# Kernel tuning notes

Hardware: AMD Instinct MI355X
Metric: run time of the kernel (lower is better)

## Reference

```python
import jax, jax.numpy as jnp
import numpy as np

B, L, D, H, NBLK, NNBR = 256, 200, 128, 2, 2, 10
ITEMS, USERS = 100001, 50001
NEG = -1e9
EPS = 1e-8


def layernorm(x, s, b):
    mu = jnp.mean(x, axis=-1, keepdims=True)
    var = jnp.mean(jnp.square(x - mu), axis=-1, keepdims=True)
    return (x - mu) / jnp.sqrt(var + EPS) * s + b


def mha(q, kv, Wqkv_i, bqkv_i, Wo_i, bo_i, causal_bias):
    # torch.nn.MultiheadAttention math (eval mode), Q from layernormed seq, K=V=seq
    d = q.shape[-1]
    hd = d // H
    Wq, Wk, Wv = Wqkv_i[:d], Wqkv_i[d:2 * d], Wqkv_i[2 * d:]
    bq, bk, bv = bqkv_i[:d], bqkv_i[d:2 * d], bqkv_i[2 * d:]
    Q = (q @ Wq.T + bq).reshape(q.shape[0], q.shape[1], H, hd)
    K = (kv @ Wk.T + bk).reshape(q.shape[0], q.shape[1], H, hd)
    V = (kv @ Wv.T + bv).reshape(q.shape[0], q.shape[1], H, hd)
    scores = jnp.einsum('bqhd,bkhd->bhqk', Q, K) / jnp.sqrt(jnp.float32(hd))
    attn = jax.nn.softmax(scores + causal_bias, axis=-1)
    out = jnp.einsum('bhqk,bkhd->bqhd', attn, V).reshape(q.shape[0], q.shape[1], d)
    return out @ Wo_i.T + bo_i


def setup_inputs() -> dict:
    key = jax.random.key(0)
    ks = jax.random.split(key, 12)
    s = 0.02
    inp = {
        'log_seqs': jax.random.randint(ks[0], (B, L), 0, ITEMS),
        'nbr_idx': jax.random.randint(ks[1], (B, L, NNBR), 0, USERS),
        'item_emb': jax.random.normal(ks[2], (ITEMS, D), jnp.float32) * s,
        'user_emb': jax.random.normal(ks[3], (USERS, D), jnp.float32) * s,
        'pos_emb': jax.random.normal(ks[4], (L, D), jnp.float32) * s,
        'attn_ln_s': jnp.ones((NBLK, D), jnp.float32),
        'attn_ln_b': jnp.zeros((NBLK, D), jnp.float32),
        'Wqkv': jax.random.normal(ks[5], (NBLK, 3 * D, D), jnp.float32) * s,
        'bqkv': jnp.zeros((NBLK, 3 * D), jnp.float32),
        'Wo': jax.random.normal(ks[6], (NBLK, D, D), jnp.float32) * s,
        'bo': jnp.zeros((NBLK, D), jnp.float32),
        'ffn_ln_s': jnp.ones((NBLK, D), jnp.float32),
        'ffn_ln_b': jnp.zeros((NBLK, D), jnp.float32),
        'W1': jax.random.normal(ks[7], (NBLK, D, D), jnp.float32) * s,
        'b1': jnp.zeros((NBLK, D), jnp.float32),
        'W2': jax.random.normal(ks[8], (NBLK, D, D), jnp.float32) * s,
        'b2': jnp.zeros((NBLK, D), jnp.float32),
        'last_ln_s': jnp.ones((D,), jnp.float32),
        'last_ln_b': jnp.zeros((D,), jnp.float32),
        'iui_ln_s': jnp.ones((D,), jnp.float32),
        'iui_ln_b': jnp.zeros((D,), jnp.float32),
    }
    return inp


def reference(log_seqs, nbr_idx, item_emb, user_emb, pos_emb, attn_ln_s, attn_ln_b,
              Wqkv, bqkv, Wo, bo, ffn_ln_s, ffn_ln_b, W1, b1, W2, b2,
              last_ln_s, last_ln_b, iui_ln_s, iui_ln_b):
    d = item_emb.shape[1]
    seqlen = log_seqs.shape[1]
    # SASRec log2feats core (eval mode, dropout disabled)
    seqs = item_emb[log_seqs] * jnp.sqrt(jnp.float32(d)) + pos_emb[None, :seqlen]
    tl_mask = (log_seqs != 0)[..., None].astype(seqs.dtype)
    seqs = seqs * tl_mask
    causal_bias = jnp.where(jnp.tril(jnp.ones((seqlen, seqlen), bool)), 0.0, NEG)
    for i in range(Wqkv.shape[0]):
        q = layernorm(seqs, attn_ln_s[i], attn_ln_b[i])
        seqs = q + mha(q, seqs, Wqkv[i], bqkv[i], Wo[i], bo[i], causal_bias)
        x = layernorm(seqs, ffn_ln_s[i], ffn_ln_b[i])
        # PointWiseFeedForward: 1x1 conv == linear, residual inside
        h = jax.nn.relu(x @ W1[i].T + b1[i]) @ W2[i].T + b2[i]
        seqs = (h + x) * tl_mask
    feats = layernorm(seqs, last_ln_s, last_ln_b)
    # iui meta-path: gather up to 10 user neighbors per item, masked attention aggregation
    qn = item_emb[log_seqs]                       # [B,L,D]
    kn = user_emb[nbr_idx]                        # [B,L,N,D]
    sc = jnp.einsum('bld,blnd->bln', qn, kn) / jnp.sqrt(jnp.float32(d))
    sc = jnp.where(nbr_idx != 0, sc, NEG)
    w = jax.nn.softmax(sc, axis=-1)
    agg = jnp.einsum('bln,blnd->bld', w, kn)
    nbr = layernorm(agg + qn, iui_ln_s, iui_ln_b)
    return feats + nbr
```

## Files before the change

kernel.cpp:

```cpp
#include <hip/hip_runtime.h>
#include <hip/hip_bf16.h>

#define L_SEQ 200
#define DIM 128
#define NROWS (256*200)

typedef __attribute__((ext_vector_type(8))) short bf16x8;
typedef __attribute__((ext_vector_type(4))) float f32x4;

__device__ __forceinline__ float wave_sum(float v){
  #pragma unroll
  for (int o = 32; o; o >>= 1) v += __shfl_xor(v, o);
  return v;
}
__device__ __forceinline__ short f2bf(float f){
  union { float f; unsigned u; } x; x.f = f;
  unsigned r = x.u + 0x7fffu + ((x.u >> 16) & 1u);
  return (short)(r >> 16);
}
__device__ __forceinline__ float bf2f(unsigned short u){
  union { unsigned u; float f; } x; x.u = ((unsigned)u) << 16;
  return x.f;
}

__global__ void cvt_all_kernel(const float* __restrict__ Wqkv, const float* __restrict__ Wo,
                               const float* __restrict__ W1, const float* __restrict__ W2,
                               short* __restrict__ dst){
  int i = blockIdx.x*256 + threadIdx.x;
  if (i >= 49152) return;
  const float* src; int off;
  if (i < 24576)      { src = Wqkv; off = i; }
  else if (i < 32768) { src = Wo;   off = i - 24576; }
  else if (i < 40960) { src = W1;   off = i - 32768; }
  else                { src = W2;   off = i - 40960; }
  float4 v = ((const float4*)src)[off];
  short4 s; s.x = f2bf(v.x); s.y = f2bf(v.y); s.z = f2bf(v.z); s.w = f2bf(v.w);
  ((short4*)dst)[i] = s;
}

__global__ void cvt4_kernel(const float* __restrict__ src, short* __restrict__ dst, int n4){
  int i = blockIdx.x*256 + threadIdx.x;
  if (i < n4) {
    float4 v = ((const float4*)src)[i];
    short4 s; s.x = f2bf(v.x); s.y = f2bf(v.y); s.z = f2bf(v.z); s.w = f2bf(v.w);
    ((short4*)dst)[i] = s;
  }
}

__global__ __launch_bounds__(256) void embed_ln_kernel(
    const int* __restrict__ lsq, const float* __restrict__ item,
    const float* __restrict__ pos, const float* __restrict__ s, const float* __restrict__ b,
    short* __restrict__ seqs_b, short* __restrict__ lnq_b, short* __restrict__ qn_b){
  int wave = threadIdx.x >> 6, lane = threadIdx.x & 63;
  size_t r = (size_t)blockIdx.x*4 + wave;
  int it = lsq[r];
  float2 iv = ((const float2*)(item + (size_t)it*DIM))[lane];
  float2 p = ((const float2*)(pos + (r % L_SEQ)*DIM))[lane];
  short2 qv; qv.x = f2bf(iv.x); qv.y = f2bf(iv.y);
  ((short2*)(qn_b + r*DIM))[lane] = qv;
  float vx = 0.f, vy = 0.f;
  if (it) {
    vx = iv.x * 11.313708498984761f + p.x;
    vy = iv.y * 11.313708498984761f + p.y;
  }
  short2 sv; sv.x = f2bf(vx); sv.y = f2bf(vy);
  ((short2*)(seqs_b + r*DIM))[lane] = sv;
  float mu = wave_sum(vx + vy) * (1.f/DIM);
  float dx = vx - mu, dy = vy - mu;
  float var = wave_sum(dx*dx + dy*dy) * (1.f/DIM);
  float inv = 1.f / sqrtf(var + 1e-8f);
  float2 sc = ((const float2*)s)[lane];
  float2 bc = ((const float2*)b)[lane];
  short2 ov; ov.x = f2bf(dx*inv*sc.x + bc.x); ov.y = f2bf(dy*inv*sc.y + bc.y);
  ((short2*)(lnq_b + r*DIM))[lane] = ov;
}

#define MLP_MFMA(accv) do { \
  _Pragma("unroll") \
  for (int kc = 0; kc < 4; ++kc) { \
    bf16x8 af[4], bfr[2]; \
    _Pragma("unroll") \
    for (int mf = 0; mf < 4; ++mf) { \
      int rr = mbase + mf*16 + col; \
      int byt = (rr*256 + kc*64 + g*16) ^ ((rr & 7) << 4); \
      af[mf] = *(bf16x8*)(AsB + byt); \
    } \
    _Pragma("unroll") \
    for (int nf = 0; nf < 2; ++nf) { \
      int rr = nbase + nf*16 + col; \
      int byt = (rr*256 + kc*64 + g*16) ^ ((rr & 7) << 4); \
      bfr[nf] = *(bf16x8*)(BsB + byt); \
    } \
    _Pragma("unroll") \
    for (int mf = 0; mf < 4; ++mf) \
      _Pragma("unroll") \
      for (int nf = 0; nf < 2; ++nf) \
        accv[mf][nf] = __builtin_amdgcn_mfma_f32_16x16x32_bf16(af[mf], bfr[nf], accv[mf][nf], 0, 0, 0); \
  } \
} while(0)

#define LN_REDUCE(accv) do { \
  _Pragma("unroll") \
  for (int mf = 0; mf < 4; ++mf) { \
    _Pragma("unroll") \
    for (int r = 0; r < 4; ++r) { \
      float s1 = accv[mf][0][r] + accv[mf][1][r]; \
      float s2 = accv[mf][0][r]*accv[mf][0][r] + accv[mf][1][r]*accv[mf][1][r]; \
      _Pragma("unroll") \
      for (int o = 1; o <= 8; o <<= 1) { s1 += __shfl_xor(s1, o); s2 += __shfl_xor(s2, o); } \
      if (col == 0) { int rL = mbase + mf*16 + g*4 + r; redP[0][wn][rL] = s1; redP[1][wn][rL] = s2; } \
    } \
  } \
  __syncthreads(); \
  if (t < 128) { \
    float s1 = redP[0][0][t] + redP[0][1][t] + redP[0][2][t] + redP[0][3][t]; \
    float s2 = redP[1][0][t] + redP[1][1][t] + redP[1][2][t] + redP[1][3][t]; \
    float mu_ = s1 * (1.f/DIM); \
    float var_ = s2 * (1.f/DIM) - mu_*mu_; \
    muA[t] = mu_; invA[t] = 1.f / sqrtf(var_ + 1e-8f); \
  } \
  __syncthreads(); \
} while(0)

__global__ __launch_bounds__(512) void qkv_kernel(
    const short* __restrict__ lnq, const short* __restrict__ seqs,
    const short* __restrict__ Wb, const float* __restrict__ bias,
    short* __restrict__ C){
  __shared__ short As[16384];
  __shared__ short Bs[16384];
  char* AsB = (char*)As; char* BsB = (char*)Bs;
  const int row0 = blockIdx.y * 128, col0 = blockIdx.x * 128;
  const int t = threadIdx.x;
  const short* Ap = (blockIdx.x == 0) ? lnq : seqs;

  #pragma unroll
  for (int i = 0; i < 4; ++i) {
    int flat = t*8 + i*4096;
    int rr = flat >> 7, cc = flat & 127;
    bf16x8 a8 = *(const bf16x8*)(Ap + (size_t)(row0 + rr)*128 + cc);
    int byt = (rr*256 + cc*2) ^ ((rr & 7) << 4);
    *(bf16x8*)(AsB + byt) = a8;
    bf16x8 b8 = *(const bf16x8*)(Wb + (size_t)(col0 + rr)*128 + cc);
    *(bf16x8*)(BsB + byt) = b8;
  }
  __syncthreads();

  const int w = t >> 6, l = t & 63;
  const int wm = w >> 2, wn = w & 3;
  const int col = l & 15, g = l >> 4;
  const int mbase = wm*64, nbase = wn*32;

  f32x4 acc[4][2];
  #pragma unroll
  for (int mf = 0; mf < 4; ++mf)
    #pragma unroll
    for (int nf = 0; nf < 2; ++nf) { f32x4 z = {0.f,0.f,0.f,0.f}; acc[mf][nf] = z; }
  MLP_MFMA(acc);

  float biasv[2];
  #pragma unroll
  for (int nf = 0; nf < 2; ++nf) biasv[nf] = bias[col0 + nbase + nf*16 + col];
  const float qs = (blockIdx.x == 0) ? 0.125f : 1.f;
  #pragma unroll
  for (int mf = 0; mf < 4; ++mf)
    #pragma unroll
    for (int r = 0; r < 4; ++r) {
      int rr = row0 + mbase + mf*16 + g*4 + r;
      #pragma unroll
      for (int nf = 0; nf < 2; ++nf) {
        int cc = col0 + nbase + nf*16 + col;
        float v = (acc[mf][nf][r] + biasv[nf]) * qs;
        C[(size_t)rr*384 + cc] = f2bf(v);
      }
    }
}

template<int WRITE_C>
__global__ __launch_bounds__(512) void mlp_kernel(
    const short* __restrict__ qkvQ, const short* __restrict__ resq,
    const short* __restrict__ wo_b, const float* __restrict__ bo,
    const float* __restrict__ ffnS, const float* __restrict__ ffnB,
    const short* __restrict__ w1_b, const float* __restrict__ b1,
    const short* __restrict__ w2_b, const float* __restrict__ b2,
    const int* __restrict__ lsq,
    short* __restrict__ C,
    const float* __restrict__ lnS2, const float* __restrict__ lnB2,
    short* __restrict__ lnOut){
  __shared__ short As[16384];
  __shared__ short Bs[16384];
  __shared__ float redP[2][4][128];
  __shared__ float muA[128], invA[128];
  char* AsB = (char*)As; char* BsB = (char*)Bs;
  const int row0 = blockIdx.x * 128;
  const int t = threadIdx.x;

  #pragma unroll
  for (int i = 0; i < 4; ++i) {
    int flat = t*8 + i*4096;
    int rr = flat >> 7, cc = flat & 127;
    bf16x8 a8 = *(const bf16x8*)(qkvQ + (size_t)(row0 + rr)*384 + cc);
    int byt = (rr*256 + cc*2) ^ ((rr & 7) << 4);
    *(bf16x8*)(AsB + byt) = a8;
    bf16x8 b8 = *(const bf16x8*)(wo_b + (size_t)rr*128 + cc);
    *(bf16x8*)(BsB + byt) = b8;
  }
  __syncthreads();

  const int w = t >> 6, l = t & 63;
  const int wm = w >> 2, wn = w & 3;
  const int col = l & 15, g = l >> 4;
  const int mbase = wm*64, nbase = wn*32;

  f32x4 acc[4][2];
  #pragma unroll
  for (int mf = 0; mf < 4; ++mf)
    #pragma unroll
    for (int nf = 0; nf < 2; ++nf) { f32x4 z = {0.f,0.f,0.f,0.f}; acc[mf][nf] = z; }
  MLP_MFMA(acc);

  float bov[2];
  #pragma unroll
  for (int nf = 0; nf < 2; ++nf) bov[nf] = bo[nbase + nf*16 + col];
  #pragma unroll
  for (int mf = 0; mf < 4; ++mf)
    #pragma unroll
    for (int r = 0; r < 4; ++r) {
      int rL = mbase + mf*16 + g*4 + r;
      #pragma unroll
      for (int nf = 0; nf < 2; ++nf) {
        int cL = nbase + nf*16 + col;
        acc[mf][nf][r] += bov[nf] + bf2f(((const unsigned short*)resq)[(size_t)(row0 + rL)*DIM + cL]);
      }
    }
  LN_REDUCE(acc);

  float xv[4][2][4];
  #pragma unroll
  for (int mf = 0; mf < 4; ++mf)
    #pragma unroll
    for (int r = 0; r < 4; ++r) {
      int rL = mbase + mf*16 + g*4 + r;
      float mu = muA[rL], inv = invA[rL];
      #pragma unroll
      for (int nf = 0; nf < 2; ++nf) {
        int cL = nbase + nf*16 + col;
        float lnv = (acc[mf][nf][r] - mu)*inv*ffnS[cL] + ffnB[cL];
        xv[mf][nf][r] = lnv;
        int byt = (rL*256 + cL*2) ^ ((rL & 7) << 4);
        *(short*)(AsB + byt) = f2bf(lnv);
      }
    }
  #pragma unroll
  for (int i = 0; i < 4; ++i) {
    int flat = t*8 + i*4096;
    int rr = flat >> 7, cc = flat & 127;
    bf16x8 b8 = *(const bf16x8*)(w1_b + (size_t)rr*128 + cc);
    int byt = (rr*256 + cc*2) ^ ((rr & 7) << 4);
    *(bf16x8*)(BsB + byt) = b8;
  }
  __syncthreads();

  #pragma unroll
  for (int mf = 0; mf < 4; ++mf)
    #pragma unroll
    for (int nf = 0; nf < 2; ++nf) { f32x4 z = {0.f,0.f,0.f,0.f}; acc[mf][nf] = z; }
  MLP_MFMA(acc);
  __syncthreads();

  float b1v[2];
  #pragma unroll
  for (int nf = 0; nf < 2; ++nf) b1v[nf] = b1[nbase + nf*16 + col];
  #pragma unroll
  for (int mf = 0; mf < 4; ++mf)
    #pragma unroll
    for (int r = 0; r < 4; ++r) {
      int rL = mbase + mf*16 + g*4 + r;
      #pragma unroll
      for (int nf = 0; nf < 2; ++nf) {
        int cL = nbase + nf*16 + col;
        float h = fmaxf(acc[mf][nf][r] + b1v[nf], 0.f);
        int byt = (rL*256 + cL*2) ^ ((rL & 7) << 4);
        *(short*)(AsB + byt) = f2bf(h);
      }
    }
  #pragma unroll
  for (int i = 0; i < 4; ++i) {
    int flat = t*8 + i*4096;
    int rr = flat >> 7, cc = flat & 127;
    bf16x8 b8 = *(const bf16x8*)(w2_b + (size_t)rr*128 + cc);
    int byt = (rr*256 + cc*2) ^ ((rr & 7) << 4);
    *(bf16x8*)(BsB + byt) = b8;
  }
  __syncthreads();

  #pragma unroll
  for (int mf = 0; mf < 4; ++mf)
    #pragma unroll
    for (int nf = 0; nf < 2; ++nf) { f32x4 z = {0.f,0.f,0.f,0.f}; acc[mf][nf] = z; }
  MLP_MFMA(acc);

  float b2v[2];
  #pragma unroll
  for (int nf = 0; nf < 2; ++nf) b2v[nf] = b2[nbase + nf*16 + col];
  #pragma unroll
  for (int mf = 0; mf < 4; ++mf)
    #pragma unroll
    for (int r = 0; r < 4; ++r) {
      int rL = mbase + mf*16 + g*4 + r;
      bool zr = (lsq[row0 + rL] == 0);
      #pragma unroll
      for (int nf = 0; nf < 2; ++nf) {
        float v = acc[mf][nf][r] + b2v[nf] + xv[mf][nf][r];
        if (zr) v = 0.f;
        acc[mf][nf][r] = v;
      }
    }
  LN_REDUCE(acc);
  #pragma unroll
  for (int mf = 0; mf < 4; ++mf)
    #pragma unroll
    for (int r = 0; r < 4; ++r) {
      int rL = mbase + mf*16 + g*4 + r;
      float mu = muA[rL], inv = invA[rL];
      #pragma unroll
      for (int nf = 0; nf < 2; ++nf) {
        int cL = nbase + nf*16 + col;
        float v = acc[mf][nf][r];
        float lnv = (v - mu)*inv*lnS2[cL] + lnB2[cL];
        lnOut[(size_t)(row0 + rL)*DIM + cL] = f2bf(lnv);
        if (WRITE_C) C[(size_t)(row0 + rL)*DIM + cL] = f2bf(v);
      }
    }
}

__global__ __launch_bounds__(512) void attn_kernel(short* __restrict__ qkv){
  __shared__ short Ks[224*64];
  __shared__ short Vt[64*224];
  __shared__ short Ps[8][16*232];
  const int b = blockIdx.x >> 1, h = blockIdx.x & 1;
  short* base = qkv + (size_t)b*L_SEQ*384 + h*64;
  const short* baseK = base + 128;
  const short* baseV = base + 256;
  const int t = threadIdx.x;
  char* KsB = (char*)Ks;
  char* VtB = (char*)Vt;

  for (int idx = t; idx < 224*8; idx += 512) {
    int row = idx >> 3, c8 = idx & 7;
    bf16x8 kv = {0,0,0,0,0,0,0,0}, vv = {0,0,0,0,0,0,0,0};
    if (row < L_SEQ) {
      kv = *(const bf16x8*)(baseK + (size_t)row*384 + c8*8);
      vv = *(const bf16x8*)(baseV + (size_t)row*384 + c8*8);
    }
    int kbyte = (row*128 + c8*16) ^ ((row & 7) << 4);
    *(bf16x8*)(KsB + kbyte) = kv;
    #pragma unroll
    for (int e = 0; e < 8; ++e) {
      int d = c8*8 + e;
      int vbyte = (d*448 + row*2) ^ ((d & 7) << 4);
      *(short*)(VtB + vbyte) = vv[e];
    }
  }
  __syncthreads();

  const int w = t >> 6, l = t & 63;
  const int col = l & 15, g = l >> 4, g4 = g * 4;
  char* PB = (char*)Ps[w];

  const int ntiles = (w < 5) ? 2 : 1;
  for (int j = 0; j < ntiles; ++j) {
    const int qt = (j == 0) ? w : 12 - w;
    bf16x8 qf[2];
    {
      int gr = qt*16 + col;
      #pragma unroll
      for (int c = 0; c < 2; ++c) {
        bf16x8 q = {0,0,0,0,0,0,0,0};
        if (gr < L_SEQ) q = *(const bf16x8*)(base + (size_t)gr*384 + c*32 + g*8);
        qf[c] = q;
      }
    }
    f32x4 sc[13];
    #pragma unroll
    for (int kt = 0; kt < 13; ++kt) {
      if (kt <= qt) {
        f32x4 a = {0.f,0.f,0.f,0.f};
        #pragma unroll
        for (int c = 0; c < 2; ++c) {
          int row = kt*16 + col;
          int byt = (row*128 + c*64 + g*16) ^ ((row & 7) << 4);
          bf16x8 kf = *(bf16x8*)(KsB + byt);
          a = __builtin_amdgcn_mfma_f32_16x16x32_bf16(qf[c], kf, a, 0, 0, 0);
        }
        sc[kt] = a;
      }
    }
    float m[4] = {-1e30f,-1e30f,-1e30f,-1e30f};
    #pragma unroll
    for (int kt = 0; kt < 13; ++kt) {
      if (kt <= qt) {
        #pragma unroll
        for (int r = 0; r < 4; ++r) {
          bool ok = (kt < qt) || (col <= g4 + r);
          if (!ok) sc[kt][r] = -1e30f;
          m[r] = fmaxf(m[r], sc[kt][r]);
        }
      }
    }
    #pragma unroll
    for (int r = 0; r < 4; ++r) {
      #pragma unroll
      for (int o = 1; o <= 8; o <<= 1) m[r] = fmaxf(m[r], __shfl_xor(m[r], o));
    }
    float s[4] = {0.f,0.f,0.f,0.f};
    #pragma unroll
    for (int kt = 0; kt < 13; ++kt) {
      if (kt <= qt) {
        #pragma unroll
        for (int r = 0; r < 4; ++r) {
          float e = __expf(sc[kt][r] - m[r]);
          sc[kt][r] = e;
          s[r] += e;
        }
      }
    }
    float inv[4];
    #pragma unroll
    for (int r = 0; r < 4; ++r) {
      #pragma unroll
      for (int o = 1; o <= 8; o <<= 1) s[r] += __shfl_xor(s[r], o);
      inv[r] = 1.f / s[r];
    }
    #pragma unroll
    for (int kt = 0; kt < 13; ++kt) {
      if (kt <= qt) {
        #pragma unroll
        for (int r = 0; r < 4; ++r)
          *(short*)(PB + ((g4 + r)*232 + kt*16 + col)*2) = f2bf(sc[kt][r]);
      } else if (kt == qt + 1) {
        #pragma unroll
        for (int r = 0; r < 4; ++r)
          *(short*)(PB + ((g4 + r)*232 + kt*16 + col)*2) = 0;
      }
    }
    #pragma unroll
    for (int r = 0; r < 4; ++r)
      *(short*)(PB + ((g4 + r)*232 + 208 + col)*2) = 0;
    asm volatile("s_waitcnt lgkmcnt(0)" ::: "memory");
    f32x4 o4[4];
    #pragma unroll
    for (int nt = 0; nt < 4; ++nt) { f32x4 z = {0.f,0.f,0.f,0.f}; o4[nt] = z; }
    const int kcmax = (qt*16 + 15) >> 5;
    #pragma unroll
    for (int kc = 0; kc < 7; ++kc) {
      if (kc <= kcmax) {
        bf16x8 pf = *(bf16x8*)(PB + col*464 + kc*64 + g*16);
        #pragma unroll
        for (int nt = 0; nt < 4; ++nt) {
          int d = nt*16 + col;
          int byt = (d*448 + kc*64 + g*16) ^ ((d & 7) << 4);
          bf16x8 vf = *(bf16x8*)(VtB + byt);
          o4[nt] = __builtin_amdgcn_mfma_f32_16x16x32_bf16(pf, vf, o4[nt], 0, 0, 0);
        }
      }
    }
    #pragma unroll
    for (int nt = 0; nt < 4; ++nt)
      #pragma unroll
      for (int r = 0; r < 4; ++r) {
        int qr = qt*16 + g4 + r;
        if (qr < L_SEQ) base[(size_t)qr*384 + nt*16 + col] = f2bf(o4[nt][r] * inv[r]);
      }
  }
}

__global__ __launch_bounds__(256) void final_kernel(
    const short* __restrict__ feats_b, const short* __restrict__ qn_b,
    const int* __restrict__ nbr, const short* __restrict__ user_b,
    const float* __restrict__ is_, const float* __restrict__ ib,
    float* __restrict__ out){
  int wave = threadIdx.x >> 6, lane = threadIdx.x & 63;
  int half = lane >> 5, sl = lane & 31;
  size_t r = (size_t)blockIdx.x*8 + wave*2 + half;

  int idxs[10];
  #pragma unroll
  for (int n = 0; n < 10; ++n) idxs[n] = nbr[r*10 + n];
  ushort4 kv4[10];
  #pragma unroll
  for (int n = 0; n < 10; ++n)
    kv4[n] = ((const ushort4*)(user_b + (size_t)idxs[n]*DIM))[sl];
  ushort4 fv = ((const ushort4*)(feats_b + r*DIM))[sl];
  ushort4 qv4 = ((const ushort4*)(qn_b + r*DIM))[sl];

  float q0 = bf2f(qv4.x), q1 = bf2f(qv4.y), q2 = bf2f(qv4.z), q3 = bf2f(qv4.w);
  float kn[10][4]; float scn[10];
  #pragma unroll
  for (int n = 0; n < 10; ++n) {
    kn[n][0] = bf2f(kv4[n].x); kn[n][1] = bf2f(kv4[n].y);
    kn[n][2] = bf2f(kv4[n].z); kn[n][3] = bf2f(kv4[n].w);
    float p = q0*kn[n][0] + q1*kn[n][1] + q2*kn[n][2] + q3*kn[n][3];
    #pragma unroll
    for (int o = 1; o <= 16; o <<= 1) p += __shfl_xor(p, o);
    scn[n] = idxs[n] ? p * 0.08838834764831845f : -1.0e9f;
  }
  float m = scn[0];
  #pragma unroll
  for (int n = 1; n < 10; ++n) m = fmaxf(m, scn[n]);
  float w[10], sum = 0.f;
  #pragma unroll
  for (int n = 0; n < 10; ++n) { w[n] = expf(scn[n] - m); sum += w[n]; }
  float invs = 1.f / sum;
  float a0 = 0.f, a1 = 0.f, a2 = 0.f, a3 = 0.f;
  #pragma unroll
  for (int n = 0; n < 10; ++n) {
    a0 += w[n]*kn[n][0]; a1 += w[n]*kn[n][1]; a2 += w[n]*kn[n][2]; a3 += w[n]*kn[n][3];
  }
  a0 = a0*invs + q0;
  a1 = a1*invs + q1;
  a2 = a2*invs + q2;
  a3 = a3*invs + q3;
  float s1 = a0 + a1 + a2 + a3;
  #pragma unroll
  for (int o = 1; o <= 16; o <<= 1) s1 += __shfl_xor(s1, o);
  float mu2 = s1 * (1.f/DIM);
  float d0 = a0 - mu2, d1 = a1 - mu2, d2 = a2 - mu2, d3 = a3 - mu2;
  float sq = d0*d0 + d1*d1 + d2*d2 + d3*d3;
  #pragma unroll
  for (int o = 1; o <= 16; o <<= 1) sq += __shfl_xor(sq, o);
  float inv2 = 1.f / sqrtf(sq * (1.f/DIM) + 1e-8f);
  float f0 = bf2f(fv.x), f1 = bf2f(fv.y), f2 = bf2f(fv.z), f3 = bf2f(fv.w);
  float4 isc = ((const float4*)is_)[sl], ibc = ((const float4*)ib)[sl];
  float4 o;
  o.x = f0 + d0*inv2*isc.x + ibc.x;
  o.y = f1 + d1*inv2*isc.y + ibc.y;
  o.z = f2 + d2*inv2*isc.z + ibc.z;
  o.w = f3 + d3*inv2*isc.w + ibc.w;
  ((float4*)(out + r*DIM))[sl] = o;
}

extern "C" void kernel_launch(void* const* d_in, const int* in_sizes, int n_in,
                              void* d_out, int out_size, void* d_ws, size_t ws_size,
                              hipStream_t stream) {
  const int*   lsq    = (const int*)d_in[0];
  const int*   nbr    = (const int*)d_in[1];
  const float* item   = (const float*)d_in[2];
  const float* user   = (const float*)d_in[3];
  const float* pos    = (const float*)d_in[4];
  const float* attn_s = (const float*)d_in[5];
  const float* attn_b = (const float*)d_in[6];
  const float* Wqkv   = (const float*)d_in[7];
  const float* bqkv   = (const float*)d_in[8];
  const float* Wo     = (const float*)d_in[9];
  const float* bo     = (const float*)d_in[10];
  const float* ffn_s  = (const float*)d_in[11];
  const float* ffn_b  = (const float*)d_in[12];
  const float* W1     = (const float*)d_in[13];
  const float* b1     = (const float*)d_in[14];
  const float* W2     = (const float*)d_in[15];
  const float* b2     = (const float*)d_in[16];
  const float* last_s = (const float*)d_in[17];
  const float* last_b = (const float*)d_in[18];
  const float* iui_s  = (const float*)d_in[19];
  const float* iui_b  = (const float*)d_in[20];
  float* out = (float*)d_out;

  const int N = NROWS;
  short* seqs_b = (short*)d_ws;
  short* lnq_b  = seqs_b + (size_t)N*DIM;
  short* qkv_b  = lnq_b  + (size_t)N*DIM;
  short* wqkv_b = qkv_b  + (size_t)N*384;
  short* wo_b   = wqkv_b + 2*384*128;
  short* w1_b   = wo_b   + 2*128*128;
  short* w2_b   = w1_b   + 2*128*128;
  short* user_b = w2_b   + 2*128*128;
  short* qn_b   = user_b + (size_t)50001*DIM + 64;

  cvt_all_kernel<<<192, 256, 0, stream>>>(Wqkv, Wo, W1, W2, wqkv_b);
  cvt4_kernel<<<(50001*DIM/4 + 255)/256, 256, 0, stream>>>(user, user_b, 50001*DIM/4);

  embed_ln_kernel<<<N/4, 256, 0, stream>>>(lsq, item, pos, attn_s, attn_b,
                                           seqs_b, lnq_b, qn_b);

  for (int i = 0; i < 2; ++i) {
    qkv_kernel<<<dim3(3, N/128), 512, 0, stream>>>(
        lnq_b, seqs_b, wqkv_b + (size_t)i*384*128, bqkv + i*384, qkv_b);
    attn_kernel<<<256*2, 512, 0, stream>>>(qkv_b);
    if (i == 0) {
      mlp_kernel<1><<<N/128, 512, 0, stream>>>(
          qkv_b, lnq_b, wo_b, bo, ffn_s, ffn_b,
          w1_b, b1, w2_b, b2, lsq,
          seqs_b, attn_s + DIM, attn_b + DIM, lnq_b);
    } else {
      mlp_kernel<0><<<N/128, 512, 0, stream>>>(
          qkv_b, lnq_b, wo_b + 128*128, bo + DIM, ffn_s + DIM, ffn_b + DIM,
          w1_b + 128*128, b1 + DIM, w2_b + 128*128, b2 + DIM, lsq,
          nullptr, last_s, last_b, lnq_b);
    }
  }

  final_kernel<<<N/8, 256, 0, stream>>>(lnq_b, qn_b, nbr, user_b,
                                        iui_s, iui_b, out);
}
```

Before: 210.6 us.

## Merge prep kernels into one launch and reuse seqs tile across K/V panels

```diff
diff --git a/kernel.cpp b/kernel.cpp
--- a/kernel.cpp
+++ b/kernel.cpp
@@ -4,6 +4,12 @@
 #define L_SEQ 200
 #define DIM 128
 #define NROWS (256*200)
+
+#define W4 49152
+#define U4 (50001*DIM/4)
+#define WBLK 192
+#define UBLK ((U4 + 255)/256)
+#define EBLK (NROWS/4)
 
 typedef __attribute__((ext_vector_type(8))) short bf16x8;
 typedef __attribute__((ext_vector_type(4))) float f32x4;
@@ -23,36 +29,43 @@
   return x.f;
 }
 
-__global__ void cvt_all_kernel(const float* __restrict__ Wqkv, const float* __restrict__ Wo,
-                               const float* __restrict__ W1, const float* __restrict__ W2,
-                               short* __restrict__ dst){
-  int i = blockIdx.x*256 + threadIdx.x;
-  if (i >= 49152) return;
-  const float* src; int off;
-  if (i < 24576)      { src = Wqkv; off = i; }
-  else if (i < 32768) { src = Wo;   off = i - 24576; }
-  else if (i < 40960) { src = W1;   off = i - 32768; }
-  else                { src = W2;   off = i - 40960; }
-  float4 v = ((const float4*)src)[off];
-  short4 s; s.x = f2bf(v.x); s.y = f2bf(v.y); s.z = f2bf(v.z); s.w = f2bf(v.w);
-  ((short4*)dst)[i] = s;
-}
-
-__global__ void cvt4_kernel(const float* __restrict__ src, short* __restrict__ dst, int n4){
-  int i = blockIdx.x*256 + threadIdx.x;
-  if (i < n4) {
-    float4 v = ((const float4*)src)[i];
-    short4 s; s.x = f2bf(v.x); s.y = f2bf(v.y); s.z = f2bf(v.z); s.w = f2bf(v.w);
-    ((short4*)dst)[i] = s;
-  }
-}
-
-__global__ __launch_bounds__(256) void embed_ln_kernel(
+__global__ __launch_bounds__(256) void prep_kernel(
+    const float* __restrict__ Wqkv, const float* __restrict__ Wo,
+    const float* __restrict__ W1, const float* __restrict__ W2,
+    short* __restrict__ wdst,
+    const float* __restrict__ user, short* __restrict__ user_b,
     const int* __restrict__ lsq, const float* __restrict__ item,
-    const float* __restrict__ pos, const float* __restrict__ s, const float* __restrict__ b,
+    const float* __restrict__ pos,
+    const float* __restrict__ s, const float* __restrict__ b,
     short* __restrict__ seqs_b, short* __restrict__ lnq_b, short* __restrict__ qn_b){
+  int bid = blockIdx.x;
+  if (bid < WBLK) {
+    int i = bid*256 + threadIdx.x;
+    if (i < W4) {
+      const float* src; int off;
+      if (i < 24576)      { src = Wqkv; off = i; }
+      else if (i < 32768) { src = Wo;   off = i - 24576; }
+      else if (i < 40960) { src = W1;   off = i - 32768; }
+      else                { src = W2;   off = i - 40960; }
+      float4 v = ((const float4*)src)[off];
+      short4 sv; sv.x = f2bf(v.x); sv.y = f2bf(v.y); sv.z = f2bf(v.z); sv.w = f2bf(v.w);
+      ((short4*)wdst)[i] = sv;
+    }
+    return;
+  }
+  bid -= WBLK;
+  if (bid < UBLK) {
+    int i = bid*256 + threadIdx.x;
+    if (i < U4) {
+      float4 v = ((const float4*)user)[i];
+      short4 sv; sv.x = f2bf(v.x); sv.y = f2bf(v.y); sv.z = f2bf(v.z); sv.w = f2bf(v.w);
+      ((short4*)user_b)[i] = sv;
+    }
+    return;
+  }
+  bid -= UBLK;
   int wave = threadIdx.x >> 6, lane = threadIdx.x & 63;
-  size_t r = (size_t)blockIdx.x*4 + wave;
+  size_t r = (size_t)bid*4 + wave;
   int it = lsq[r];
   float2 iv = ((const float2*)(item + (size_t)it*DIM))[lane];
   float2 p = ((const float2*)(pos + (r % L_SEQ)*DIM))[lane];
@@ -129,9 +142,12 @@
   __shared__ short As[16384];
   __shared__ short Bs[16384];
   char* AsB = (char*)As; char* BsB = (char*)Bs;
-  const int row0 = blockIdx.y * 128, col0 = blockIdx.x * 128;
+  const int row0 = blockIdx.y * 128;
   const int t = threadIdx.x;
-  const short* Ap = (blockIdx.x == 0) ? lnq : seqs;
+  const bool isQ = (blockIdx.x == 0);
+  const short* Ap = isQ ? lnq : seqs;
+  const int npan = isQ ? 1 : 2;
+  const int colbase = isQ ? 0 : 128;
 
   #pragma unroll
   for (int i = 0; i < 4; ++i) {
@@ -140,39 +156,50 @@
     bf16x8 a8 = *(const bf16x8*)(Ap + (size_t)(row0 + rr)*128 + cc);
     int byt = (rr*256 + cc*2) ^ ((rr & 7) << 4);
     *(bf16x8*)(AsB + byt) = a8;
-    bf16x8 b8 = *(const bf16x8*)(Wb + (size_t)(col0 + rr)*128 + cc);
-    *(bf16x8*)(BsB + byt) = b8;
-  }
-  __syncthreads();
+  }
 
   const int w = t >> 6, l = t & 63;
   const int wm = w >> 2, wn = w & 3;
   const int col = l & 15, g = l >> 4;
   const int mbase = wm*64, nbase = wn*32;
-
-  f32x4 acc[4][2];
-  #pragma unroll
-  for (int mf = 0; mf < 4; ++mf)
-    #pragma unroll
-    for (int nf = 0; nf < 2; ++nf) { f32x4 z = {0.f,0.f,0.f,0.f}; acc[mf][nf] = z; }
-  MLP_MFMA(acc);
-
-  float biasv[2];
-  #pragma unroll
-  for (int nf = 0; nf < 2; ++nf) biasv[nf] = bias[col0 + nbase + nf*16 + col];
-  const float qs = (blockIdx.x == 0) ? 0.125f : 1.f;
-  #pragma unroll
-  for (int mf = 0; mf < 4; ++mf)
-    #pragma unroll
-    for (int r = 0; r < 4; ++r) {
-      int rr = row0 + mbase + mf*16 + g*4 + r;
-      #pragma unroll
-      for (int nf = 0; nf < 2; ++nf) {
-        int cc = col0 + nbase + nf*16 + col;
-        float v = (acc[mf][nf][r] + biasv[nf]) * qs;
-        C[(size_t)rr*384 + cc] = f2bf(v);
-      }
-    }
+  const float qs = isQ ? 0.125f : 1.f;
+
+  for (int p = 0; p < npan; ++p) {
+    const int col0 = colbase + p*128;
+    #pragma unroll
+    for (int i = 0; i < 4; ++i) {
+      int flat = t*8 + i*4096;
+      int rr = flat >> 7, cc = flat & 127;
+      bf16x8 b8 = *(const bf16x8*)(Wb + (size_t)(col0 + rr)*128 + cc);
+      int byt = (rr*256 + cc*2) ^ ((rr & 7) << 4);
+      *(bf16x8*)(BsB + byt) = b8;
+    }
+    __syncthreads();
+
+    f32x4 acc[4][2];
+    #pragma unroll
+    for (int mf = 0; mf < 4; ++mf)
+      #pragma unroll
+      for (int nf = 0; nf < 2; ++nf) { f32x4 z = {0.f,0.f,0.f,0.f}; acc[mf][nf] = z; }
+    MLP_MFMA(acc);
+
+    float biasv[2];
+    #pragma unroll
+    for (int nf = 0; nf < 2; ++nf) biasv[nf] = bias[col0 + nbase + nf*16 + col];
+    #pragma unroll
+    for (int mf = 0; mf < 4; ++mf)
+      #pragma unroll
+      for (int r = 0; r < 4; ++r) {
+        int rr = row0 + mbase + mf*16 + g*4 + r;
+        #pragma unroll
+        for (int nf = 0; nf < 2; ++nf) {
+          int cc = col0 + nbase + nf*16 + col;
+          float v = (acc[mf][nf][r] + biasv[nf]) * qs;
+          C[(size_t)rr*384 + cc] = f2bf(v);
+        }
+      }
+    __syncthreads();
+  }
 }
 
 template<int WRITE_C>
@@ -576,14 +603,14 @@
   short* user_b = w2_b   + 2*128*128;
   short* qn_b   = user_b + (size_t)50001*DIM + 64;
 
-  cvt_all_kernel<<<192, 256, 0, stream>>>(Wqkv, Wo, W1, W2, wqkv_b);
-  cvt4_kernel<<<(50001*DIM/4 + 255)/256, 256, 0, stream>>>(user, user_b, 50001*DIM/4);
-
-  embed_ln_kernel<<<N/4, 256, 0, stream>>>(lsq, item, pos, attn_s, attn_b,
-                                           seqs_b, lnq_b, qn_b);
+  prep_kernel<<<WBLK + UBLK + EBLK, 256, 0, stream>>>(
+      Wqkv, Wo, W1, W2, wqkv_b,
+      user, user_b,
+      lsq, item, pos, attn_s, attn_b,
+      seqs_b, lnq_b, qn_b);
 
   for (int i = 0; i < 2; ++i) {
-    qkv_kernel<<<dim3(3, N/128), 512, 0, stream>>>(
+    qkv_kernel<<<dim3(2, N/128), 512, 0, stream>>>(
         lnq_b, seqs_b, wqkv_b + (size_t)i*384*128, bqkv + i*384, qkv_b);
     attn_kernel<<<256*2, 512, 0, stream>>>(qkv_b);
     if (i == 0) {
```

Measured after the change: 221.9 us. 1.05x slower.
